# Optimization experiments

Measured on AMD Instinct MI355X. Metric: run time of the kernel, lower is better.

The kernel has to match this reference:

```python
import jax, jax.numpy as jnp
import numpy as np

CAPACITY_FACTOR = 1.25
AUX_W = 0.1
Z_W = 0.001


def setup_inputs() -> dict:
    key = jax.random.key(0)
    k0, k1, k2, k3 = jax.random.split(key, 4)
    B, T, C, E, H = 4, 2048, 896, 3, 3584
    x = jax.random.normal(k0, (B, T, C), dtype=jnp.float32)
    Wr = jax.random.normal(k1, (E, C), dtype=jnp.float32) * 0.02   # router Linear(C->E)
    W1 = jax.random.normal(k2, (E, H, C), dtype=jnp.float32) * 0.02  # per-expert Linear(C->H)
    W2 = jax.random.normal(k3, (E, C, H), dtype=jnp.float32) * 0.02  # per-expert Linear(H->C)
    return {"x": x, "Wr": Wr, "W1": W1, "W2": W2}


def reference(x, Wr, W1, W2):
    B, T, C = x.shape
    E = Wr.shape[0]
    N = B * T
    capacity = int(CAPACITY_FACTOR * N / E)  # static

    # --- router ---
    logits = jnp.einsum('btc,ec->bte', x, Wr)                      # [B,T,E]
    z_loss = Z_W * jnp.mean(jax.nn.logsumexp(logits, axis=-1) ** 2)
    probs = jax.nn.softmax(logits, axis=-1)
    pf = probs.reshape(N, E)
    expert_index = jnp.argmax(pf, axis=-1)                          # top-1
    mask = jax.nn.one_hot(expert_index, E, dtype=x.dtype)           # [N,E]

    # capacity-limited dispatch: per expert keep top-`capacity` tokens by router prob.
    # (When an expert has <= capacity tokens this keeps all of them, matching the
    #  torch reference's two branches.)
    scores = jnp.where(mask > 0, pf, -jnp.inf).T                    # [E,N]
    _, top_idx = jax.lax.top_k(scores, capacity)                    # [E,capacity]
    disp = jnp.zeros((E, N), dtype=x.dtype).at[jnp.arange(E)[:, None], top_idx].set(1.0)
    dispatch = (disp * mask.T).T                                    # [N,E], kills -inf picks

    gates = pf * dispatch
    gates = gates / (jnp.sum(gates, axis=-1, keepdims=True) + 1e-6)  # [N,E]

    aux_loss = AUX_W * jnp.sum(dispatch.mean(axis=0) * pf.mean(axis=0)) * E

    # --- experts (dense over tokens, gated combine; dropout in eval = identity) ---
    xf = x.reshape(N, C)
    h = jax.nn.gelu(jnp.einsum('nc,ehc->neh', xf, W1), approximate=False)  # [N,E,H]
    y = jnp.einsum('neh,ech->nec', h, W2)                                   # [N,E,C]
    out = xf + jnp.einsum('nec,ne->nc', y, gates)                           # residual + combine
    return out.reshape(B, T, C), aux_loss + z_loss
```

## Files before the change

kernel.cpp:

```cpp
#include <hip/hip_runtime.h>
#include <stdint.h>

#define B_ 4
#define T_ 2048
#define C_ 896
#define E_ 3
#define H_ 3584
#define N_ 8192
#define CVB 256
#define NRT 14

typedef __attribute__((ext_vector_type(8))) short short8;
typedef __attribute__((ext_vector_type(4))) float f32x4;

#define OFF_XB   ((size_t)0)
#define OFF_W1B  ((size_t)14680064)
#define OFF_W2B  ((size_t)33947648)
#define OFF_HB   ((size_t)53215232)
#define OFF_PERM ((size_t)111935488)
#define OFF_EID  ((size_t)112033792)
#define OFF_GATE ((size_t)112066560)
#define OFF_PBUF ((size_t)112099328)
#define OFF_LSE2 ((size_t)112197632)
#define OFF_CNT  ((size_t)112230400)
#define OFF_P    OFF_XB

static __device__ __forceinline__ unsigned short f2b(float f) {
  union { float f; unsigned u; } v; v.f = f;
  unsigned r = v.u + 0x7FFFu + ((v.u >> 16) & 1u);
  return (unsigned short)(r >> 16);
}

static __device__ __forceinline__ float gelu_fast(float v) {
  float u = 0.7978845608f * v * fmaf(0.044715f * v, v, 1.0f);
  u = fminf(u, 20.0f);
  float t = __expf(2.0f * u);
  return v * t * __builtin_amdgcn_rcpf(t + 1.0f);
}

static __device__ __forceinline__ int xcd_chunk(int lin, int total) {
  int q = total >> 3, r = total & 7;
  int xcd = lin & 7, idx = lin >> 3;
  return (xcd < r ? xcd * (q + 1) : r * (q + 1) + (xcd - r) * q) + idx;
}

static __device__ __forceinline__ void grp_decode(int t, int rt, int ncol, int RG, int CG,
                                                  int* rowt, int* colt) {
  const int fullbands = rt / RG;
  const int bandsz = RG * ncol;
  if (t < fullbands * bandsz) {
    int band = t / bandsz, tr = t % bandsz;
    int cg = tr / (CG * RG), r2 = tr % (CG * RG);
    *rowt = band * RG + r2 / CG;
    *colt = cg * CG + r2 % CG;
  } else {
    int t2 = t - fullbands * bandsz;
    int tail = rt - fullbands * RG;
    int cg = t2 / (CG * tail), r2 = t2 % (CG * tail);
    *rowt = fullbands * RG + r2 / CG;
    *colt = cg * CG + r2 % CG;
  }
}

static __device__ __forceinline__ void cvt_stride(const float* __restrict__ src,
                                                  unsigned short* __restrict__ dst,
                                                  int n4, int bid, int nblk) {
  const int stride = nblk * blockDim.x;
  for (int i = bid * blockDim.x + threadIdx.x; i < n4; i += stride) {
    float4 v = reinterpret_cast<const float4*>(src)[i];
    ushort4 o;
    o.x = f2b(v.x); o.y = f2b(v.y); o.z = f2b(v.z); o.w = f2b(v.w);
    reinterpret_cast<ushort4*>(dst)[i] = o;
  }
}

__global__ __launch_bounds__(256) void router_kernel(
    const float* __restrict__ x, const float* __restrict__ Wr,
    unsigned short* __restrict__ xb,
    int* __restrict__ eid, float* __restrict__ gate,
    float* __restrict__ pbuf, float* __restrict__ lse2,
    const float* __restrict__ W1, unsigned short* __restrict__ w1b) {
  if (blockIdx.x >= N_ / 8) {
    cvt_stride(W1, w1b, E_ * H_ * C_ / 4, blockIdx.x - N_ / 8, 1024);
    return;
  }
  const int tid = threadIdx.x;
  const int sub = tid & 31;
  const int n = blockIdx.x * 8 + (tid >> 5);
  const float4* xr = reinterpret_cast<const float4*>(x + (size_t)n * C_);
  ushort4* xw = reinterpret_cast<ushort4*>(xb + (size_t)n * C_);
  const float4* w0p = reinterpret_cast<const float4*>(Wr + 0 * C_);
  const float4* w1p = reinterpret_cast<const float4*>(Wr + 1 * C_);
  const float4* w2p = reinterpret_cast<const float4*>(Wr + 2 * C_);
  float s0 = 0.f, s1 = 0.f, s2 = 0.f;
#pragma unroll
  for (int j = 0; j < 7; ++j) {
    const int idx = sub + 32 * j;
    float4 v = xr[idx];
    ushort4 o;
    o.x = f2b(v.x); o.y = f2b(v.y); o.z = f2b(v.z); o.w = f2b(v.w);
    xw[idx] = o;
    float4 a = w0p[idx], b = w1p[idx], c = w2p[idx];
    s0 += v.x * a.x + v.y * a.y + v.z * a.z + v.w * a.w;
    s1 += v.x * b.x + v.y * b.y + v.z * b.z + v.w * b.w;
    s2 += v.x * c.x + v.y * c.y + v.z * c.z + v.w * c.w;
  }
#pragma unroll
  for (int off = 16; off > 0; off >>= 1) {
    s0 += __shfl_xor(s0, off);
    s1 += __shfl_xor(s1, off);
    s2 += __shfl_xor(s2, off);
  }
  if (sub == 0) {
    float m = fmaxf(s0, fmaxf(s1, s2));
    float e0 = expf(s0 - m), e1 = expf(s1 - m), e2 = expf(s2 - m);
    float sum = e0 + e1 + e2;
    float p0 = e0 / sum, p1 = e1 / sum, p2 = e2 / sum;
    int am = 0; float best = s0;
    if (s1 > best) { best = s1; am = 1; }
    if (s2 > best) { best = s2; am = 2; }
    float pa = (am == 0) ? p0 : ((am == 1) ? p1 : p2);
    eid[n] = am;
    gate[n] = pa / (pa + 1e-6f);
    pbuf[n * 3 + 0] = p0; pbuf[n * 3 + 1] = p1; pbuf[n * 3 + 2] = p2;
    float lse = m + logf(sum);
    lse2[n] = lse * lse;
  }
}

__global__ __launch_bounds__(1024) void scatter_kernel(const int* __restrict__ eid,
                                                       int* __restrict__ counts,
                                                       int* __restrict__ perm) {
  __shared__ int hist[E_];
  __shared__ int base[E_];
  const int t = threadIdx.x;
  const int n = blockIdx.x * 1024 + t;
  if (t < E_) hist[t] = 0;
  __syncthreads();
  int e = eid[n];
  int l = atomicAdd(&hist[e], 1);
  __syncthreads();
  if (t < E_) base[t] = atomicAdd(&counts[t], hist[t]);
  __syncthreads();
  perm[e * N_ + base[e] + l] = n;
}

#define STAGE_TILE()                                                                    \
  do {                                                                                  \
    _Pragma("unroll")                                                                   \
    for (int i_ = 0; i_ < 4; ++i_) {                                                    \
      __builtin_amdgcn_global_load_lds(                                                 \
          (const __attribute__((address_space(1))) void*)pA_[i_],                       \
          (__attribute__((address_space(3))) void*)&shA[(wv * 4 + i_) * 512], 16, 0, 0); \
    }                                                                                   \
    _Pragma("unroll")                                                                   \
    for (int i_ = 0; i_ < 2; ++i_) {                                                    \
      __builtin_amdgcn_global_load_lds(                                                 \
          (const __attribute__((address_space(1))) void*)pB_[i_],                       \
          (__attribute__((address_space(3))) void*)&shB[(wv * 2 + i_) * 512], 16, 0, 0); \
    }                                                                                   \
    _Pragma("unroll")                                                                   \
    for (int i_ = 0; i_ < 4; ++i_) { pA_[i_] += 64; }                                   \
    _Pragma("unroll")                                                                   \
    for (int i_ = 0; i_ < 2; ++i_) { pB_[i_] += 64; }                                   \
  } while (0)

#define COMPUTE_TILE()                                                                  \
  do {                                                                                  \
    _Pragma("unroll")                                                                   \
    for (int kk = 0; kk < 2; ++kk) {                                                    \
      const int sl_ = ((kk * 4 + (lane >> 4)) ^ (lane & 7)) * 8;                        \
      short8 af[4], bfv[4];                                                             \
      _Pragma("unroll")                                                                 \
      for (int m = 0; m < 4; ++m) {                                                     \
        int row = wm * 64 + m * 16 + (lane & 15);                                       \
        af[m] = *reinterpret_cast<const short8*>(&shA[row * 64 + sl_]);                 \
      }                                                                                 \
      _Pragma("unroll")                                                                 \
      for (int nn = 0; nn < 4; ++nn) {                                                  \
        int row = wn * 64 + nn * 16 + (lane & 15);                                      \
        bfv[nn] = *reinterpret_cast<const short8*>(&shB[row * 64 + sl_]);               \
      }                                                                                 \
      _Pragma("unroll")                                                                 \
      for (int m = 0; m < 4; ++m)                                                       \
        _Pragma("unroll")                                                               \
        for (int nn = 0; nn < 4; ++nn)                                                  \
          acc[m][nn] = __builtin_amdgcn_mfma_f32_16x16x32_bf16(af[m], bfv[nn], acc[m][nn], 0, 0, 0); \
    }                                                                                   \
  } while (0)

#define K_LOOP(NT)                                                                      \
  do {                                                                                  \
    for (int kt = 0; kt < (NT); ++kt) {                                                 \
      STAGE_TILE();                                                                     \
      __syncthreads();                                                                  \
      COMPUTE_TILE();                                                                   \
      __syncthreads();                                                                  \
    }                                                                                   \
  } while (0)

__global__ __launch_bounds__(512) void gemm1_kernel(
    const unsigned short* __restrict__ xb,
    const unsigned short* __restrict__ w1b,
    unsigned short* __restrict__ h,
    const int* __restrict__ perm, const int* __restrict__ counts,
    const float* __restrict__ W2, unsigned short* __restrict__ w2b) {
  if (blockIdx.x < CVB) {
    cvt_stride(W2, w2b, E_ * C_ * H_ / 4, blockIdx.x, CVB);
    return;
  }
  const int c0 = counts[0], c1 = counts[1], c2 = counts[2];
  const int rt0 = (c0 + 255) >> 8, rt1 = (c1 + 255) >> 8, rt2 = (c2 + 255) >> 8;
  const int n0 = rt0 * 28, n1 = rt1 * 28, n2 = rt2 * 28;
  const int total = n0 + n1 + n2;
  const int lin = blockIdx.x - CVB;
  if (lin >= total) return;
  const int wgid = xcd_chunk(lin, total);
  int e, rem, rt_e, count;
  if (wgid < n0)            { e = 0; rem = wgid;           rt_e = rt0; count = c0; }
  else if (wgid < n0 + n1)  { e = 1; rem = wgid - n0;      rt_e = rt1; count = c1; }
  else                      { e = 2; rem = wgid - n0 - n1; rt_e = rt2; count = c2; }
  int rowt, colt;
  grp_decode(rem, rt_e, 28, 4, 7, &rowt, &colt);
  const int row0 = rowt * 256;
  const int col0 = colt * 128;
  const int tid = threadIdx.x, lane = tid & 63, wv = tid >> 6;
  const int wm = wv >> 1, wn = wv & 1;
  const int* permE = perm + e * N_;
  const unsigned short* w1e = w1b + (size_t)e * H_ * C_;

  __shared__ __align__(16) unsigned short shA[256 * 64];
  __shared__ __align__(16) unsigned short shB[128 * 64];

  f32x4 acc[4][4];
#pragma unroll
  for (int i = 0; i < 4; ++i)
#pragma unroll
    for (int j = 0; j < 4; ++j) acc[i][j] = (f32x4){0.f, 0.f, 0.f, 0.f};

  const int cc = (((lane & 7) ^ (lane >> 3))) * 8;
  const unsigned short* pA_[4];
  const unsigned short* pB_[2];
#pragma unroll
  for (int i = 0; i < 4; ++i) {
    int s = row0 + wv * 32 + i * 8 + (lane >> 3);
    if (s >= count) s = count - 1;
    pA_[i] = xb + (size_t)permE[s] * C_ + cc;
  }
#pragma unroll
  for (int i = 0; i < 2; ++i) {
    int r = wv * 16 + i * 8 + (lane >> 3);
    pB_[i] = w1e + (size_t)(col0 + r) * C_ + cc;
  }

  K_LOOP(C_ / 64);

#pragma unroll
  for (int m = 0; m < 4; ++m) {
    int rbase = wm * 64 + m * 16 + (lane >> 4) * 4;
#pragma unroll
    for (int i = 0; i < 4; ++i) {
      int s = row0 + rbase + i;
      if (s < count) {
        int ntok = permE[s];
#pragma unroll
        for (int nn = 0; nn < 4; ++nn) {
          int col = col0 + wn * 64 + nn * 16 + (lane & 15);
          h[(size_t)ntok * H_ + col] = f2b(gelu_fast(acc[m][nn][i]));
        }
      }
    }
  }
}

__global__ __launch_bounds__(512) void gemm2_kernel(
    const unsigned short* __restrict__ h,
    const unsigned short* __restrict__ w2b,
    const float* __restrict__ x,
    const float* __restrict__ gate,
    float* __restrict__ out, float* __restrict__ P,
    const int* __restrict__ perm, const int* __restrict__ counts) {
  const int c0 = counts[0], c1 = counts[1], c2 = counts[2];
  const int rt0 = (c0 + 255) >> 8, rt1 = (c1 + 255) >> 8, rt2 = (c2 + 255) >> 8;
  const int n0 = rt0 * 14, n1 = rt1 * 14, n2 = rt2 * 14;
  const int total = n0 + n1 + n2;
  const int lin = blockIdx.x;
  if (lin >= total) return;
  const int wgid = xcd_chunk(lin, total);
  int e, rem, rt_e, count;
  if (wgid < n0)            { e = 0; rem = wgid;           rt_e = rt0; count = c0; }
  else if (wgid < n0 + n1)  { e = 1; rem = wgid - n0;      rt_e = rt1; count = c1; }
  else                      { e = 2; rem = wgid - n0 - n1; rt_e = rt2; count = c2; }
  int rowt, c14;
  grp_decode(rem, rt_e, 14, 2, 7, &rowt, &c14);
  const int ks = c14 / 7;
  const int colt = c14 % 7;
  const int row0 = rowt * 256;
  const int col0 = colt * 128;
  const int kbase = ks * (H_ / 2);
  const int tid = threadIdx.x, lane = tid & 63, wv = tid >> 6;
  const int wm = wv >> 1, wn = wv & 1;
  const int* permE = perm + e * N_;
  const unsigned short* w2e = w2b + (size_t)e * C_ * H_;

  __shared__ __align__(16) unsigned short shA[256 * 64];
  __shared__ __align__(16) unsigned short shB[128 * 64];

  f32x4 acc[4][4];
#pragma unroll
  for (int i = 0; i < 4; ++i)
#pragma unroll
    for (int j = 0; j < 4; ++j) acc[i][j] = (f32x4){0.f, 0.f, 0.f, 0.f};

  const int cc = (((lane & 7) ^ (lane >> 3))) * 8;
  const unsigned short* pA_[4];
  const unsigned short* pB_[2];
#pragma unroll
  for (int i = 0; i < 4; ++i) {
    int s = row0 + wv * 32 + i * 8 + (lane >> 3);
    if (s >= count) s = count - 1;
    pA_[i] = h + (size_t)permE[s] * H_ + kbase + cc;
  }
#pragma unroll
  for (int i = 0; i < 2; ++i) {
    int r = wv * 16 + i * 8 + (lane >> 3);
    pB_[i] = w2e + (size_t)(col0 + r) * H_ + kbase + cc;
  }

  K_LOOP((H_ / 2) / 64);

#pragma unroll
  for (int m = 0; m < 4; ++m) {
    int rbase = wm * 64 + m * 16 + (lane >> 4) * 4;
#pragma unroll
    for (int i = 0; i < 4; ++i) {
      int s = row0 + rbase + i;
      if (s < count) {
        int ntok = permE[s];
        float g = gate[ntok];
        if (ks == 0) {
#pragma unroll
          for (int nn = 0; nn < 4; ++nn) {
            int col = col0 + wn * 64 + nn * 16 + (lane & 15);
            out[(size_t)ntok * C_ + col] = x[(size_t)ntok * C_ + col] + g * acc[m][nn][i];
          }
        } else {
#pragma unroll
          for (int nn = 0; nn < 4; ++nn) {
            int col = col0 + wn * 64 + nn * 16 + (lane & 15);
            P[(size_t)ntok * C_ + col] = g * acc[m][nn][i];
          }
        }
      }
    }
  }
}

__global__ __launch_bounds__(256) void combine_kernel(
    float* __restrict__ out, const float* __restrict__ P, int n4,
    const float* __restrict__ lse2, const float* __restrict__ pbuf,
    const int* __restrict__ eid) {
  int stride = gridDim.x * blockDim.x;
  for (int i = blockIdx.x * blockDim.x + threadIdx.x; i < n4; i += stride) {
    float4 a = reinterpret_cast<float4*>(out)[i];
    float4 b = reinterpret_cast<const float4*>(P)[i];
    a.x += b.x; a.y += b.y; a.z += b.z; a.w += b.w;
    reinterpret_cast<float4*>(out)[i] = a;
  }
  if (blockIdx.x == 0) {
    __shared__ float sh[7][256];
    float a = 0.f, p0 = 0.f, p1 = 0.f, p2 = 0.f, c0 = 0.f, c1 = 0.f, c2 = 0.f;
    for (int n = threadIdx.x; n < N_; n += 256) {
      a += lse2[n];
      p0 += pbuf[n * 3 + 0]; p1 += pbuf[n * 3 + 1]; p2 += pbuf[n * 3 + 2];
      int e = eid[n];
      c0 += (e == 0); c1 += (e == 1); c2 += (e == 2);
    }
    sh[0][threadIdx.x] = a;
    sh[1][threadIdx.x] = p0; sh[2][threadIdx.x] = p1; sh[3][threadIdx.x] = p2;
    sh[4][threadIdx.x] = c0; sh[5][threadIdx.x] = c1; sh[6][threadIdx.x] = c2;
    for (int s = 128; s > 0; s >>= 1) {
      __syncthreads();
      if (threadIdx.x < (unsigned)s)
#pragma unroll
        for (int q = 0; q < 7; ++q) sh[q][threadIdx.x] += sh[q][threadIdx.x + s];
    }
    if (threadIdx.x == 0) {
      const float invN = 1.0f / (float)N_;
      float z = 0.001f * (sh[0][0] * invN);
      float aux = 0.1f * (float)E_ *
                  (sh[4][0] * invN * sh[1][0] * invN +
                   sh[5][0] * invN * sh[2][0] * invN +
                   sh[6][0] * invN * sh[3][0] * invN);
      out[(size_t)N_ * C_] = z + aux;
    }
  }
}

extern "C" void kernel_launch(void* const* d_in, const int* in_sizes, int n_in,
                              void* d_out, int out_size, void* d_ws, size_t ws_size,
                              hipStream_t stream) {
  const float* x  = (const float*)d_in[0];
  const float* Wr = (const float*)d_in[1];
  const float* W1 = (const float*)d_in[2];
  const float* W2 = (const float*)d_in[3];
  float* out = (float*)d_out;
  char* ws = (char*)d_ws;

  unsigned short* xb  = (unsigned short*)(ws + OFF_XB);
  unsigned short* w1b = (unsigned short*)(ws + OFF_W1B);
  unsigned short* w2b = (unsigned short*)(ws + OFF_W2B);
  unsigned short* hb  = (unsigned short*)(ws + OFF_HB);
  int*   perm  = (int*)(ws + OFF_PERM);
  int*   eid   = (int*)(ws + OFF_EID);
  float* gate  = (float*)(ws + OFF_GATE);
  float* pbuf  = (float*)(ws + OFF_PBUF);
  float* lse2  = (float*)(ws + OFF_LSE2);
  int*   counts = (int*)(ws + OFF_CNT);
  float* P     = (float*)(ws + OFF_P);

  hipMemsetAsync(counts, 0, E_ * sizeof(int), stream);

  router_kernel<<<2048, 256, 0, stream>>>(x, Wr, xb, eid, gate, pbuf, lse2, W1, w1b);
  scatter_kernel<<<N_ / 1024, 1024, 0, stream>>>(eid, counts, perm);

  gemm1_kernel<<<CVB + NRT * 28 * E_, 512, 0, stream>>>(xb, w1b, hb, perm, counts, W2, w2b);
  gemm2_kernel<<<NRT * 14 * E_, 512, 0, stream>>>(hb, w2b, x, gate, out, P, perm, counts);
  combine_kernel<<<2048, 256, 0, stream>>>(out, P, N_ * C_ / 4, lse2, pbuf, eid);
}
```

Before: 181.5 us.

## Drop split-K in gemm2 and remove combine pass, move loss to own kernel

gemm2 no longer splits the H reduction into two halves. Each workgroup now runs the full K loop and writes the final residual plus gated output directly. This removes the partial-sum buffer P and the full-size combine kernel that read and rewrote all of out. The loss reduction moves to a small single-block kernel launched after scatter. The trade-off is half as many gemm2 workgroups, each with twice the K length, which may leave CUs underused.

```diff
diff --git a/kernel.cpp b/kernel.cpp
--- a/kernel.cpp
+++ b/kernel.cpp
@@ -23,7 +23,6 @@
 #define OFF_PBUF ((size_t)112099328)
 #define OFF_LSE2 ((size_t)112197632)
 #define OFF_CNT  ((size_t)112230400)
-#define OFF_P    OFF_XB
 
 static __device__ __forceinline__ unsigned short f2b(float f) {
   union { float f; unsigned u; } v; v.f = f;
@@ -143,6 +142,38 @@
   if (t < E_) base[t] = atomicAdd(&counts[t], hist[t]);
   __syncthreads();
   perm[e * N_ + base[e] + l] = n;
+}
+
+__global__ __launch_bounds__(256) void loss_kernel(const float* __restrict__ lse2,
+                                                   const float* __restrict__ pbuf,
+                                                   const int* __restrict__ eid,
+                                                   float* __restrict__ out_loss) {
+  __shared__ float sh[7][256];
+  float a = 0.f, p0 = 0.f, p1 = 0.f, p2 = 0.f, c0 = 0.f, c1 = 0.f, c2 = 0.f;
+  for (int n = threadIdx.x; n < N_; n += 256) {
+    a += lse2[n];
+    p0 += pbuf[n * 3 + 0]; p1 += pbuf[n * 3 + 1]; p2 += pbuf[n * 3 + 2];
+    int e = eid[n];
+    c0 += (e == 0); c1 += (e == 1); c2 += (e == 2);
+  }
+  sh[0][threadIdx.x] = a;
+  sh[1][threadIdx.x] = p0; sh[2][threadIdx.x] = p1; sh[3][threadIdx.x] = p2;
+  sh[4][threadIdx.x] = c0; sh[5][threadIdx.x] = c1; sh[6][threadIdx.x] = c2;
+  for (int s = 128; s > 0; s >>= 1) {
+    __syncthreads();
+    if (threadIdx.x < (unsigned)s)
+#pragma unroll
+      for (int q = 0; q < 7; ++q) sh[q][threadIdx.x] += sh[q][threadIdx.x + s];
+  }
+  if (threadIdx.x == 0) {
+    const float invN = 1.0f / (float)N_;
+    float z = 0.001f * (sh[0][0] * invN);
+    float aux = 0.1f * (float)E_ *
+                (sh[4][0] * invN * sh[1][0] * invN +
+                 sh[5][0] * invN * sh[2][0] * invN +
+                 sh[6][0] * invN * sh[3][0] * invN);
+    out_loss[0] = z + aux;
+  }
 }
 
 #define STAGE_TILE()                                                                    \
@@ -278,11 +309,11 @@
     const unsigned short* __restrict__ w2b,
     const float* __restrict__ x,
     const float* __restrict__ gate,
-    float* __restrict__ out, float* __restrict__ P,
+    float* __restrict__ out,
     const int* __restrict__ perm, const int* __restrict__ counts) {
   const int c0 = counts[0], c1 = counts[1], c2 = counts[2];
   const int rt0 = (c0 + 255) >> 8, rt1 = (c1 + 255) >> 8, rt2 = (c2 + 255) >> 8;
-  const int n0 = rt0 * 14, n1 = rt1 * 14, n2 = rt2 * 14;
+  const int n0 = rt0 * 7, n1 = rt1 * 7, n2 = rt2 * 7;
   const int total = n0 + n1 + n2;
   const int lin = blockIdx.x;
   if (lin >= total) return;
@@ -291,13 +322,10 @@
   if (wgid < n0)            { e = 0; rem = wgid;           rt_e = rt0; count = c0; }
   else if (wgid < n0 + n1)  { e = 1; rem = wgid - n0;      rt_e = rt1; count = c1; }
   else                      { e = 2; rem = wgid - n0 - n1; rt_e = rt2; count = c2; }
-  int rowt, c14;
-  grp_decode(rem, rt_e, 14, 2, 7, &rowt, &c14);
-  const int ks = c14 / 7;
-  const int colt = c14 % 7;
+  int rowt, colt;
+  grp_decode(rem, rt_e, 7, 2, 7, &rowt, &colt);
   const int row0 = rowt * 256;
   const int col0 = colt * 128;
-  const int kbase = ks * (H_ / 2);
   const int tid = threadIdx.x, lane = tid & 63, wv = tid >> 6;
   const int wm = wv >> 1, wn = wv & 1;
   const int* permE = perm + e * N_;
@@ -319,15 +347,15 @@
   for (int i = 0; i < 4; ++i) {
     int s = row0 + wv * 32 + i * 8 + (lane >> 3);
     if (s >= count) s = count - 1;
-    pA_[i] = h + (size_t)permE[s] * H_ + kbase + cc;
+    pA_[i] = h + (size_t)permE[s] * H_ + cc;
   }
 #pragma unroll
   for (int i = 0; i < 2; ++i) {
     int r = wv * 16 + i * 8 + (lane >> 3);
-    pB_[i] = w2e + (size_t)(col0 + r) * H_ + kbase + cc;
-  }
-
-  K_LOOP((H_ / 2) / 64);
+    pB_[i] = w2e + (size_t)(col0 + r) * H_ + cc;
+  }
+
+  K_LOOP(H_ / 64);
 
 #pragma unroll
   for (int m = 0; m < 4; ++m) {
@@ -338,61 +366,12 @@
       if (s < count) {
         int ntok = permE[s];
         float g = gate[ntok];
-        if (ks == 0) {
-#pragma unroll
-          for (int nn = 0; nn < 4; ++nn) {
-            int col = col0 + wn * 64 + nn * 16 + (lane & 15);
-            out[(size_t)ntok * C_ + col] = x[(size_t)ntok * C_ + col] + g * acc[m][nn][i];
-          }
-        } else {
-#pragma unroll
-          for (int nn = 0; nn < 4; ++nn) {
-            int col = col0 + wn * 64 + nn * 16 + (lane & 15);
-            P[(size_t)ntok * C_ + col] = g * acc[m][nn][i];
-          }
+#pragma unroll
+        for (int nn = 0; nn < 4; ++nn) {
+          int col = col0 + wn * 64 + nn * 16 + (lane & 15);
+          out[(size_t)ntok * C_ + col] = x[(size_t)ntok * C_ + col] + g * acc[m][nn][i];
         }
       }
-    }
-  }
-}
-
-__global__ __launch_bounds__(256) void combine_kernel(
-    float* __restrict__ out, const float* __restrict__ P, int n4,
-    const float* __restrict__ lse2, const float* __restrict__ pbuf,
-    const int* __restrict__ eid) {
-  int stride = gridDim.x * blockDim.x;
-  for (int i = blockIdx.x * blockDim.x + threadIdx.x; i < n4; i += stride) {
-    float4 a = reinterpret_cast<float4*>(out)[i];
-    float4 b = reinterpret_cast<const float4*>(P)[i];
-    a.x += b.x; a.y += b.y; a.z += b.z; a.w += b.w;
-    reinterpret_cast<float4*>(out)[i] = a;
-  }
-  if (blockIdx.x == 0) {
-    __shared__ float sh[7][256];
-    float a = 0.f, p0 = 0.f, p1 = 0.f, p2 = 0.f, c0 = 0.f, c1 = 0.f, c2 = 0.f;
-    for (int n = threadIdx.x; n < N_; n += 256) {
-      a += lse2[n];
-      p0 += pbuf[n * 3 + 0]; p1 += pbuf[n * 3 + 1]; p2 += pbuf[n * 3 + 2];
-      int e = eid[n];
-      c0 += (e == 0); c1 += (e == 1); c2 += (e == 2);
-    }
-    sh[0][threadIdx.x] = a;
-    sh[1][threadIdx.x] = p0; sh[2][threadIdx.x] = p1; sh[3][threadIdx.x] = p2;
-    sh[4][threadIdx.x] = c0; sh[5][threadIdx.x] = c1; sh[6][threadIdx.x] = c2;
-    for (int s = 128; s > 0; s >>= 1) {
-      __syncthreads();
-      if (threadIdx.x < (unsigned)s)
-#pragma unroll
-        for (int q = 0; q < 7; ++q) sh[q][threadIdx.x] += sh[q][threadIdx.x + s];
-    }
-    if (threadIdx.x == 0) {
-      const float invN = 1.0f / (float)N_;
-      float z = 0.001f * (sh[0][0] * invN);
-      float aux = 0.1f * (float)E_ *
-                  (sh[4][0] * invN * sh[1][0] * invN +
-                   sh[5][0] * invN * sh[2][0] * invN +
-                   sh[6][0] * invN * sh[3][0] * invN);
-      out[(size_t)N_ * C_] = z + aux;
     }
   }
 }
@@ -417,14 +396,13 @@
   float* pbuf  = (float*)(ws + OFF_PBUF);
   float* lse2  = (float*)(ws + OFF_LSE2);
   int*   counts = (int*)(ws + OFF_CNT);
-  float* P     = (float*)(ws + OFF_P);
 
   hipMemsetAsync(counts, 0, E_ * sizeof(int), stream);
 
   router_kernel<<<2048, 256, 0, stream>>>(x, Wr, xb, eid, gate, pbuf, lse2, W1, w1b);
   scatter_kernel<<<N_ / 1024, 1024, 0, stream>>>(eid, counts, perm);
+  loss_kernel<<<1, 256, 0, stream>>>(lse2, pbuf, eid, out + (size_t)N_ * C_);
 
   gemm1_kernel<<<CVB + NRT * 28 * E_, 512, 0, stream>>>(xb, w1b, hb, perm, counts, W2, w2b);
-  gemm2_kernel<<<NRT * 14 * E_, 512, 0, stream>>>(hb, w2b, x, gate, out, P, perm, counts);
-  combine_kernel<<<2048, 256, 0, stream>>>(out, P, N_ * C_ / 4, lse2, pbuf, eid);
-}
+  gemm2_kernel<<<NRT * 7 * E_, 512, 0, stream>>>(hb, w2b, x, gate, out, perm, counts);
+}
```

Measured after the change: 193.4 us. 6.6% more time.

## Double-buffer gemm1 LDS tiles with a K=32 prefetch pipeline

Applied to the files above, without the earlier changes.

gemm1 now stages K-tiles of 32 into two LDS buffers and issues the next tile's global-to-LDS loads before computing the current one. Partial vmcnt waits let loads overlap the MFMA work, which is meant to hide the global load latency that the old load-sync-compute-sync loop exposed. Each iteration does half the MFMAs, so the loop runs twice as many times with twice as many barriers. gemm2 keeps the old single-buffer loop under renamed macros.

```diff
diff --git a/kernel.cpp b/kernel.cpp
--- a/kernel.cpp
+++ b/kernel.cpp
@@ -145,58 +145,39 @@
   perm[e * N_ + base[e] + l] = n;
 }
 
-#define STAGE_TILE()                                                                    \
+#define STAGE1D(bufA, bufB)                                                             \
   do {                                                                                  \
     _Pragma("unroll")                                                                   \
-    for (int i_ = 0; i_ < 4; ++i_) {                                                    \
+    for (int i_ = 0; i_ < 2; ++i_) {                                                    \
       __builtin_amdgcn_global_load_lds(                                                 \
           (const __attribute__((address_space(1))) void*)pA_[i_],                       \
-          (__attribute__((address_space(3))) void*)&shA[(wv * 4 + i_) * 512], 16, 0, 0); \
-    }                                                                                   \
-    _Pragma("unroll")                                                                   \
-    for (int i_ = 0; i_ < 2; ++i_) {                                                    \
-      __builtin_amdgcn_global_load_lds(                                                 \
-          (const __attribute__((address_space(1))) void*)pB_[i_],                       \
-          (__attribute__((address_space(3))) void*)&shB[(wv * 2 + i_) * 512], 16, 0, 0); \
-    }                                                                                   \
-    _Pragma("unroll")                                                                   \
-    for (int i_ = 0; i_ < 4; ++i_) { pA_[i_] += 64; }                                   \
-    _Pragma("unroll")                                                                   \
-    for (int i_ = 0; i_ < 2; ++i_) { pB_[i_] += 64; }                                   \
+          (__attribute__((address_space(3))) void*)&(bufA)[(wv * 32 + i_ * 16) * 32], 16, 0, 0); \
+    }                                                                                   \
+    __builtin_amdgcn_global_load_lds(                                                   \
+        (const __attribute__((address_space(1))) void*)pB_[0],                          \
+        (__attribute__((address_space(3))) void*)&(bufB)[(wv * 16) * 32], 16, 0, 0);    \
+    pA_[0] += 32; pA_[1] += 32; pB_[0] += 32;                                           \
   } while (0)
 
-#define COMPUTE_TILE()                                                                  \
+#define COMPUTE1D(bufA, bufB)                                                           \
   do {                                                                                  \
-    _Pragma("unroll")                                                                   \
-    for (int kk = 0; kk < 2; ++kk) {                                                    \
-      const int sl_ = ((kk * 4 + (lane >> 4)) ^ (lane & 7)) * 8;                        \
-      short8 af[4], bfv[4];                                                             \
+    const int sl_ = (((lane >> 4) ^ (lane & 3))) * 8;                                   \
+    short8 af[4], bfv[4];                                                               \
+    _Pragma("unroll")                                                                   \
+    for (int m = 0; m < 4; ++m) {                                                       \
+      int row = wm * 64 + m * 16 + (lane & 15);                                         \
+      af[m] = *reinterpret_cast<const short8*>(&(bufA)[row * 32 + sl_]);                \
+    }                                                                                   \
+    _Pragma("unroll")                                                                   \
+    for (int nn = 0; nn < 4; ++nn) {                                                    \
+      int row = wn * 64 + nn * 16 + (lane & 15);                                        \
+      bfv[nn] = *reinterpret_cast<const short8*>(&(bufB)[row * 32 + sl_]);              \
+    }                                                                                   \
+    _Pragma("unroll")                                                                   \
+    for (int m = 0; m < 4; ++m)                                                         \
       _Pragma("unroll")                                                                 \
-      for (int m = 0; m < 4; ++m) {                                                     \
-        int row = wm * 64 + m * 16 + (lane & 15);                                       \
-        af[m] = *reinterpret_cast<const short8*>(&shA[row * 64 + sl_]);                 \
-      }                                                                                 \
-      _Pragma("unroll")                                                                 \
-      for (int nn = 0; nn < 4; ++nn) {                                                  \
-        int row = wn * 64 + nn * 16 + (lane & 15);                                      \
-        bfv[nn] = *reinterpret_cast<const short8*>(&shB[row * 64 + sl_]);               \
-      }                                                                                 \
-      _Pragma("unroll")                                                                 \
-      for (int m = 0; m < 4; ++m)                                                       \
-        _Pragma("unroll")                                                               \
-        for (int nn = 0; nn < 4; ++nn)                                                  \
-          acc[m][nn] = __builtin_amdgcn_mfma_f32_16x16x32_bf16(af[m], bfv[nn], acc[m][nn], 0, 0, 0); \
-    }                                                                                   \
-  } while (0)
-
-#define K_LOOP(NT)                                                                      \
-  do {                                                                                  \
-    for (int kt = 0; kt < (NT); ++kt) {                                                 \
-      STAGE_TILE();                                                                     \
-      __syncthreads();                                                                  \
-      COMPUTE_TILE();                                                                   \
-      __syncthreads();                                                                  \
-    }                                                                                   \
+      for (int nn = 0; nn < 4; ++nn)                                                    \
+        acc[m][nn] = __builtin_amdgcn_mfma_f32_16x16x32_bf16(af[m], bfv[nn], acc[m][nn], 0, 0, 0); \
   } while (0)
 
 __global__ __launch_bounds__(512) void gemm1_kernel(
@@ -229,8 +210,8 @@
   const int* permE = perm + e * N_;
   const unsigned short* w1e = w1b + (size_t)e * H_ * C_;
 
-  __shared__ __align__(16) unsigned short shA[256 * 64];
-  __shared__ __align__(16) unsigned short shB[128 * 64];
+  __shared__ __align__(16) unsigned short shA[2][256 * 32];
+  __shared__ __align__(16) unsigned short shB[2][128 * 32];
 
   f32x4 acc[4][4];
 #pragma unroll
@@ -238,22 +219,36 @@
 #pragma unroll
     for (int j = 0; j < 4; ++j) acc[i][j] = (f32x4){0.f, 0.f, 0.f, 0.f};
 
-  const int cc = (((lane & 7) ^ (lane >> 3))) * 8;
-  const unsigned short* pA_[4];
-  const unsigned short* pB_[2];
-#pragma unroll
-  for (int i = 0; i < 4; ++i) {
-    int s = row0 + wv * 32 + i * 8 + (lane >> 3);
+  const int cc2 = (((lane & 3) ^ ((lane >> 2) & 3))) * 8;
+  const unsigned short* pA_[2];
+  const unsigned short* pB_[1];
+#pragma unroll
+  for (int i = 0; i < 2; ++i) {
+    int s = row0 + wv * 32 + i * 16 + (lane >> 2);
     if (s >= count) s = count - 1;
-    pA_[i] = xb + (size_t)permE[s] * C_ + cc;
-  }
-#pragma unroll
-  for (int i = 0; i < 2; ++i) {
-    int r = wv * 16 + i * 8 + (lane >> 3);
-    pB_[i] = w1e + (size_t)(col0 + r) * C_ + cc;
-  }
-
-  K_LOOP(C_ / 64);
+    pA_[i] = xb + (size_t)permE[s] * C_ + cc2;
+  }
+  {
+    int r = wv * 16 + (lane >> 2);
+    pB_[0] = w1e + (size_t)(col0 + r) * C_ + cc2;
+  }
+
+  const int NT = C_ / 32;
+  STAGE1D(shA[0], shB[0]);
+  int cur = 0;
+  for (int kt = 0; kt < NT; ++kt) {
+    if (kt + 1 < NT) {
+      if (cur) { STAGE1D(shA[0], shB[0]); } else { STAGE1D(shA[1], shB[1]); }
+      asm volatile("s_waitcnt vmcnt(3)" ::: "memory");
+    } else {
+      asm volatile("s_waitcnt vmcnt(0)" ::: "memory");
+    }
+    __builtin_amdgcn_s_barrier();
+    if (cur) { COMPUTE1D(shA[1], shB[1]); } else { COMPUTE1D(shA[0], shB[0]); }
+    asm volatile("" ::: "memory");
+    __builtin_amdgcn_s_barrier();
+    cur ^= 1;
+  }
 
 #pragma unroll
   for (int m = 0; m < 4; ++m) {
@@ -272,6 +267,50 @@
     }
   }
 }
+
+#define STAGE2()                                                                        \
+  do {                                                                                  \
+    _Pragma("unroll")                                                                   \
+    for (int i_ = 0; i_ < 4; ++i_) {                                                    \
+      __builtin_amdgcn_global_load_lds(                                                 \
+          (const __attribute__((address_space(1))) void*)pA_[i_],                       \
+          (__attribute__((address_space(3))) void*)&shA[(wv * 4 + i_) * 512], 16, 0, 0); \
+    }                                                                                   \
+    _Pragma("unroll")                                                                   \
+    for (int i_ = 0; i_ < 2; ++i_) {                                                    \
+      __builtin_amdgcn_global_load_lds(                                                 \
+          (const __attribute__((address_space(1))) void*)pB_[i_],                       \
+          (__attribute__((address_space(3))) void*)&shB[(wv * 2 + i_) * 512], 16, 0, 0); \
+    }                                                                                   \
+    _Pragma("unroll")                                                                   \
+    for (int i_ = 0; i_ < 4; ++i_) { pA_[i_] += 64; }                                   \
+    _Pragma("unroll")                                                                   \
+    for (int i_ = 0; i_ < 2; ++i_) { pB_[i_] += 64; }                                   \
+  } while (0)
+
+#define COMPUTE2()                                                                      \
+  do {                                                                                  \
+    _Pragma("unroll")                                                                   \
+    for (int kk = 0; kk < 2; ++kk) {                                                    \
+      const int sl_ = ((kk * 4 + (lane >> 4)) ^ (lane & 7)) * 8;                        \
+      short8 af[4], bfv[4];                                                             \
+      _Pragma("unroll")                                                                 \
+      for (int m = 0; m < 4; ++m) {                                                     \
+        int row = wm * 64 + m * 16 + (lane & 15);                                       \
+        af[m] = *reinterpret_cast<const short8*>(&shA[row * 64 + sl_]);                 \
+      }                                                                                 \
+      _Pragma("unroll")                                                                 \
+      for (int nn = 0; nn < 4; ++nn) {                                                  \
+        int row = wn * 64 + nn * 16 + (lane & 15);                                      \
+        bfv[nn] = *reinterpret_cast<const short8*>(&shB[row * 64 + sl_]);               \
+      }                                                                                 \
+      _Pragma("unroll")                                                                 \
+      for (int m = 0; m < 4; ++m)                                                       \
+        _Pragma("unroll")                                                               \
+        for (int nn = 0; nn < 4; ++nn)                                                  \
+          acc[m][nn] = __builtin_amdgcn_mfma_f32_16x16x32_bf16(af[m], bfv[nn], acc[m][nn], 0, 0, 0); \
+    }                                                                                   \
+  } while (0)
 
 __global__ __launch_bounds__(512) void gemm2_kernel(
     const unsigned short* __restrict__ h,
@@ -327,7 +366,12 @@
     pB_[i] = w2e + (size_t)(col0 + r) * H_ + kbase + cc;
   }
 
-  K_LOOP((H_ / 2) / 64);
+  for (int kt = 0; kt < (H_ / 2) / 64; ++kt) {
+    STAGE2();
+    __syncthreads();
+    COMPUTE2();
+    __syncthreads();
+  }
 
 #pragma unroll
   for (int m = 0; m < 4; ++m) {
```

After: 227.1 us. +25.1%, slower.
